# Kernel tuning notes

Measured on AMD Instinct MI355X. Metric: run time of the kernel, lower is better.

## Reference

```python
import jax, jax.numpy as jnp
import numpy as np

B, N, K, D = 16, 16384, 16, 256  # batch, num feature tokens, num slots, slot/feature dim
FEAT = 256
LN_EPS = 1e-5


def _ln(x, g, b):
    m = jnp.mean(x, -1, keepdims=True)
    v = jnp.mean((x - m) ** 2, -1, keepdims=True)
    return (x - m) * jax.lax.rsqrt(v + LN_EPS) * g + b


def setup_inputs() -> dict:
    key = jax.random.key(0)
    ks = jax.random.split(key, 18)
    s = 0.02
    return {
        "features": jax.random.normal(ks[0], (B, N, FEAT), jnp.float32),
        "slots_init": jax.random.normal(ks[1], (B, K, D), jnp.float32),
        "g_f": jnp.ones((FEAT,), jnp.float32), "b_f": jnp.zeros((FEAT,), jnp.float32),
        "g_s": jnp.ones((D,), jnp.float32), "b_s": jnp.zeros((D,), jnp.float32),
        "g_m": jnp.ones((D,), jnp.float32), "b_m": jnp.zeros((D,), jnp.float32),
        "Wq": jax.random.normal(ks[2], (D, D), jnp.float32) * s,
        "Wk": jax.random.normal(ks[3], (D, FEAT), jnp.float32) * s,
        "Wv": jax.random.normal(ks[4], (D, FEAT), jnp.float32) * s,
        "w_ih": jax.random.normal(ks[5], (3 * D, D), jnp.float32) * s,
        "w_hh": jax.random.normal(ks[6], (3 * D, D), jnp.float32) * s,
        "b_ih": jnp.zeros((3 * D,), jnp.float32),
        "b_hh": jnp.zeros((3 * D,), jnp.float32),
        "W1": jax.random.normal(ks[7], (4 * D, D), jnp.float32) * s,
        "b1": jnp.zeros((4 * D,), jnp.float32),
        "W2": jax.random.normal(ks[8], (D, 4 * D), jnp.float32) * s,
        "b2": jnp.zeros((D,), jnp.float32),
        "num_src_view": 4,
    }


def reference(features, slots_init, g_f, b_f, g_s, b_s, g_m, b_m, Wq, Wk, Wv,
              w_ih, w_hh, b_ih, b_hh, W1, b1, W2, b2, num_src_view):
    f = _ln(features, g_f, b_f)            # [B,N,FEAT]
    k = f @ Wk.T                            # [B,N,D]
    v = f @ Wv.T                            # [B,N,D]
    scale = float(D) ** -0.5                # num_head = 1, head-mean is identity

    def gru(x, h):  # PyTorch GRUCell math, batched over [B,K]
        gi = x @ w_ih.T + b_ih
        gh = h @ w_hh.T + b_hh
        ir, iz, inn = jnp.split(gi, 3, -1)
        hr, hz, hn = jnp.split(gh, 3, -1)
        r = jax.nn.sigmoid(ir + hr)
        z = jax.nn.sigmoid(iz + hz)
        n = jnp.tanh(inn + r * hn)
        return (1.0 - z) * n + z * h

    def one_iter(slots):
        q = _ln(slots, g_s, b_s) @ Wq.T                         # [B,K,D]
        logits = jnp.einsum('bkd,bnd->bkn', q, k) * scale       # [B,K,N]
        attn = jax.nn.softmax(logits, axis=1)                   # competitive over slots
        attn_wm = attn / (jnp.sum(attn, -1, keepdims=True) + 1.0)  # epsilon = 1.0
        updates = jnp.einsum('bkn,bnd->bkd', attn_wm, v)        # [B,K,D]
        h = gru(updates, slots)
        h = h + (jax.nn.relu(_ln(h, g_m, b_m) @ W1.T + b1) @ W2.T + b2)
        return h, attn

    slots = slots_init
    for _ in range(2):  # num_iter - 1 iterations with straight-through detach trick
        slots, _ = one_iter(slots)
        slots = jax.lax.stop_gradient(slots) + slots_init - jax.lax.stop_gradient(slots_init)
    slots, attn = one_iter(slots)
    return slots, attn
```

## Files before the change

kernel.cpp:

```cpp
#include <hip/hip_runtime.h>
#include <cstdint>
#include <cstddef>

#define BB    16
#define NTOK  16384
#define KS    16
#define DD    256
#define FEATN 256
#define NBLK  32
#define LN_EPS 1e-5f

typedef float        float4v __attribute__((ext_vector_type(4)));
typedef unsigned int uint4v  __attribute__((ext_vector_type(4)));
typedef unsigned int uint2v  __attribute__((ext_vector_type(2)));
typedef __bf16       bf16x8  __attribute__((ext_vector_type(8)));

__device__ __forceinline__ float bflo(unsigned u){ return __builtin_bit_cast(float, u << 16); }
__device__ __forceinline__ float bfhi(unsigned u){ return __builtin_bit_cast(float, u & 0xffff0000u); }
__device__ __forceinline__ unsigned short f2bf(float v){ __bf16 b = (__bf16)v; return __builtin_bit_cast(unsigned short, b); }
__device__ __forceinline__ float sigm(float x){ return 1.f/(1.f + __expf(-x)); }

__global__ void prep_w_kernel(const float* __restrict__ Wv, const float* __restrict__ w_ih,
                              const float* __restrict__ w_hh, const float* __restrict__ W1,
                              const float* __restrict__ W2, const float* __restrict__ Wq,
                              const float* __restrict__ Wk,
                              unsigned short* __restrict__ Wv_t, unsigned short* __restrict__ wih_t,
                              unsigned short* __restrict__ whh_t, unsigned short* __restrict__ W1_t,
                              unsigned short* __restrict__ W2_t, unsigned short* __restrict__ Wq_t,
                              unsigned short* __restrict__ Wk_b)
{
  __shared__ float tile[64][65];
  const int t = blockIdx.x, tid = threadIdx.x;
  const float* src; unsigned short* dst; int R, C, base;
  if      (t < 16)  { src = Wv;   dst = Wv_t;  R = 256;  C = 256;  base = 0;   }
  else if (t < 64)  { src = w_ih; dst = wih_t; R = 768;  C = 256;  base = 16;  }
  else if (t < 112) { src = w_hh; dst = whh_t; R = 768;  C = 256;  base = 64;  }
  else if (t < 176) { src = W1;   dst = W1_t;  R = 1024; C = 256;  base = 112; }
  else if (t < 240) { src = W2;   dst = W2_t;  R = 256;  C = 1024; base = 176; }
  else if (t < 256) { src = Wq;   dst = Wq_t;  R = 256;  C = 256;  base = 240; }
  else {
    const int t2 = t - 256;
    for (int i = tid; i < 4096; i += 256) {
      const int idx = t2*4096 + i;
      Wk_b[idx] = f2bf(Wk[idx]);
    }
    return;
  }
  const int tt = t - base;
  const int tiles_r = R >> 6;
  const int r0 = (tt % tiles_r) * 64, c0 = (tt / tiles_r) * 64;
  const int j = tid & 63, i0 = (tid >> 6) * 16;
  for (int s = 0; s < 16; ++s)
    tile[i0 + s][j] = src[(size_t)(r0 + i0 + s)*C + c0 + j];
  __syncthreads();
  for (int s = 0; s < 16; ++s) {
    const int i = i0 + s;
    dst[(size_t)(c0 + i)*R + r0 + j] = f2bf(tile[j][i]);
  }
}

__device__ __forceinline__ void lnqu_tail_p(
    const float* Vs, float* Ys, float* Qs, float* Pp, float* SUb, float* CBb,
    const float* __restrict__ g_s, const float* __restrict__ b_s,
    const unsigned short* __restrict__ Wq_t, const unsigned short* __restrict__ Wk_b,
    const float* __restrict__ g_f, const float* __restrict__ b_f,
    unsigned short* __restrict__ u_buf, float* __restrict__ su_buf, float* __restrict__ cb_buf,
    int b, int k0, int tid)
{
  const int w = tid >> 6, L = tid & 63;
  {
    const float v0 = Vs[w*256+L], v1 = Vs[w*256+64+L], v2 = Vs[w*256+128+L], v3 = Vs[w*256+192+L];
    float s = v0+v1+v2+v3;
    #pragma unroll
    for (int m = 1; m < 64; m <<= 1) s += __shfl_xor(s, m);
    const float mean = s * (1.f/DD);
    const float d0 = v0-mean, d1 = v1-mean, d2 = v2-mean, d3 = v3-mean;
    float s2 = d0*d0 + d1*d1 + d2*d2 + d3*d3;
    #pragma unroll
    for (int m = 1; m < 64; m <<= 1) s2 += __shfl_xor(s2, m);
    const float rs = rsqrtf(s2 * (1.f/DD) + LN_EPS);
    Ys[L*4+w]       = d0*rs*g_s[L]      + b_s[L];
    Ys[(64+L)*4+w]  = d1*rs*g_s[64+L]   + b_s[64+L];
    Ys[(128+L)*4+w] = d2*rs*g_s[128+L]  + b_s[128+L];
    Ys[(192+L)*4+w] = d3*rs*g_s[192+L]  + b_s[192+L];
  }
  __syncthreads();
  {
    float acc[4][4] = {};
    for (int cc = w*64; cc < w*64+64; ++cc) {
      const float4v xv = *reinterpret_cast<const float4v*>(Ys + cc*4);
      const uint2v wr = *reinterpret_cast<const uint2v*>(Wq_t + (size_t)cc*DD + 4*L);
      const float w0 = bflo(wr[0]), w1 = bfhi(wr[0]), w2 = bflo(wr[1]), w3 = bfhi(wr[1]);
      #pragma unroll
      for (int s = 0; s < 4; ++s) {
        acc[s][0] += xv[s]*w0; acc[s][1] += xv[s]*w1;
        acc[s][2] += xv[s]*w2; acc[s][3] += xv[s]*w3;
      }
    }
    #pragma unroll
    for (int s = 0; s < 4; ++s)
      *reinterpret_cast<float4v*>(Pp + (w*4+s)*256 + 4*L) = *reinterpret_cast<const float4v*>(acc[s]);
  }
  __syncthreads();
  for (int i = tid; i < 4*DD; i += 256) {
    const int kk = i >> 8, d = i & 255;
    Qs[d*4+kk] = Pp[(0*4+kk)*256+d] + Pp[(1*4+kk)*256+d] + Pp[(2*4+kk)*256+d] + Pp[(3*4+kk)*256+d];
  }
  __syncthreads();
  {
    float acc[4][4] = {};
    for (int d = w*64; d < w*64+64; ++d) {
      const float4v xv = *reinterpret_cast<const float4v*>(Qs + d*4);
      const uint2v wr = *reinterpret_cast<const uint2v*>(Wk_b + (size_t)d*DD + 4*L);
      const float w0 = bflo(wr[0]), w1 = bfhi(wr[0]), w2 = bflo(wr[1]), w3 = bfhi(wr[1]);
      #pragma unroll
      for (int s = 0; s < 4; ++s) {
        acc[s][0] += xv[s]*w0; acc[s][1] += xv[s]*w1;
        acc[s][2] += xv[s]*w2; acc[s][3] += xv[s]*w3;
      }
    }
    #pragma unroll
    for (int s = 0; s < 4; ++s)
      *reinterpret_cast<float4v*>(Pp + (w*4+s)*256 + 4*L) = *reinterpret_cast<const float4v*>(acc[s]);
  }
  __syncthreads();
  for (int i = tid; i < 4*DD; i += 256) {
    const int kk = i >> 8, cc = i & 255;
    const float qk = Pp[(0*4+kk)*256+cc] + Pp[(1*4+kk)*256+cc] + Pp[(2*4+kk)*256+cc] + Pp[(3*4+kk)*256+cc];
    const float uv = qk * g_f[cc];
    u_buf[(size_t)(b*KS + k0 + kk)*DD + cc] = f2bf(uv);
    SUb[kk*256+cc] = uv;
    CBb[kk*256+cc] = qk * b_f[cc];
  }
  __syncthreads();
  {
    float s  = SUb[w*256+L] + SUb[w*256+64+L] + SUb[w*256+128+L] + SUb[w*256+192+L];
    float cv = CBb[w*256+L] + CBb[w*256+64+L] + CBb[w*256+128+L] + CBb[w*256+192+L];
    #pragma unroll
    for (int m = 1; m < 64; m <<= 1) { s += __shfl_xor(s, m); cv += __shfl_xor(cv, m); }
    if (L == 0) { su_buf[b*KS + k0 + w] = s; cb_buf[b*KS + k0 + w] = cv; }
  }
}

__global__ void k0_kernel(const float* __restrict__ slots_init,
                          const float* __restrict__ g_s, const float* __restrict__ b_s,
                          const unsigned short* __restrict__ Wq_t, const unsigned short* __restrict__ Wk_b,
                          const float* __restrict__ g_f, const float* __restrict__ b_f,
                          unsigned short* __restrict__ u_buf, float* __restrict__ su_buf,
                          float* __restrict__ cb_buf)
{
  const int b = blockIdx.x >> 2, k0 = (blockIdx.x & 3) * 4;
  const int tid = threadIdx.x;
  __shared__ __align__(16) float Vs[4*DD];
  __shared__ __align__(16) float Ys[DD*4];
  __shared__ __align__(16) float Qs[DD*4];
  __shared__ __align__(16) float Pp[4*4*DD];
  __shared__ __align__(16) float SUb[4*DD];
  __shared__ __align__(16) float CBb[4*DD];
  for (int i = tid; i < 4*DD; i += 256)
    Vs[i] = slots_init[(size_t)(b*KS + k0)*DD + i];
  __syncthreads();
  lnqu_tail_p(Vs, Ys, Qs, Pp, SUb, CBb, g_s, b_s, Wq_t, Wk_b, g_f, b_f,
              u_buf, su_buf, cb_buf, b, k0, tid);
}

template<int MODE, int LAST>
__launch_bounds__(256, 2)
__global__ void phaseA_kernel(const float* __restrict__ feat,
                              unsigned short* __restrict__ xb, float* __restrict__ stats,
                              const unsigned short* __restrict__ u_buf,
                              const float* __restrict__ su_buf,
                              const float* __restrict__ cb_buf,
                              float* __restrict__ P_part,
                              float* __restrict__ S_part,
                              float* __restrict__ R_part,
                              float* __restrict__ attn_out)
{
  __shared__ __align__(16) unsigned int xl[4][128*36];
  __shared__ float ssh[4][16];
  __shared__ float rsh[4][16];

  const int b   = blockIdx.x / NBLK;
  const int blk = blockIdx.x - b*NBLK;
  const int tid = threadIdx.x;
  const int w = tid >> 6;
  const int l = tid & 63;
  const int c = l & 15;
  const int g = l >> 4;

  bf16x8 ufrag[8];
  {
    const bf16x8* up = reinterpret_cast<const bf16x8*>(u_buf + (size_t)(b*KS + c)*DD);
    #pragma unroll
    for (int kk = 0; kk < 8; ++kk) ufrag[kk] = up[4*kk + g];
  }
  const float su_c = su_buf[b*KS + c];
  const float cb_c = cb_buf[b*KS + c];

  float4v Pacc[16];
  #pragma unroll
  for (int t = 0; t < 16; ++t) Pacc[t] = (float4v){0.f,0.f,0.f,0.f};
  float S_acc = 0.f, R_acc = 0.f;

  unsigned int* myxl = xl[w];
  const int rbase = 8*(c>>2) + (c&3);

  for (int pass = 0; pass < 4; ++pass) {
    const int n0 = blk*(NTOK/NBLK) + pass*128 + w*32;
    float4v Ct[2];
    float m_t[2], rs_t[2];

    if constexpr (MODE == 1) {
      bf16x8 xr0[8], xr1[8];
      float2 st0, st1;
      {
        const size_t row0 = (size_t)b*NTOK + (size_t)(n0 + rbase);
        const size_t row1 = row0 + 4;
        const bf16x8* p0v = reinterpret_cast<const bf16x8*>(xb + row0*FEATN);
        const bf16x8* p1v = reinterpret_cast<const bf16x8*>(xb + row1*FEATN);
        #pragma unroll
        for (int kk = 0; kk < 8; ++kk) { xr0[kk] = p0v[4*kk + g]; xr1[kk] = p1v[4*kk + g]; }
        st0 = *reinterpret_cast<const float2*>(stats + row0*2);
        st1 = *reinterpret_cast<const float2*>(stats + row1*2);
      }
      #pragma unroll
      for (int tp = 0; tp < 2; ++tp) {
        const int nloc = rbase + 4*tp;
        float4v Cacc = (float4v){0.f,0.f,0.f,0.f};
        #pragma unroll
        for (int kk = 0; kk < 8; ++kk) {
          const bf16x8 af = tp ? xr1[kk] : xr0[kk];
          const uint4v ad = __builtin_bit_cast(uint4v, af);
          const int pb = (16*kk + 4*g)*36 + nloc;
          myxl[pb      ] = ad[0];
          myxl[pb + 36 ] = ad[1];
          myxl[pb + 72 ] = ad[2];
          myxl[pb + 108] = ad[3];
          Cacc = __builtin_amdgcn_mfma_f32_16x16x32_bf16(af, ufrag[kk], Cacc, 0, 0, 0);
        }
        m_t[tp]  = tp ? st1.x : st0.x;
        rs_t[tp] = tp ? st1.y : st0.y;
        Ct[tp]   = Cacc;
      }
    } else {
      #pragma unroll
      for (int tp = 0; tp < 2; ++tp) {
        const int nloc = rbase + 4*tp;
        const size_t row = (size_t)b*NTOK + (size_t)(n0 + nloc);
        const float* fr = feat + row*FEATN;
        float4v xf[16];
        #pragma unroll
        for (int kk = 0; kk < 8; ++kk) {
          xf[2*kk]   = *reinterpret_cast<const float4v*>(fr + 32*kk + 8*g);
          xf[2*kk+1] = *reinterpret_cast<const float4v*>(fr + 32*kk + 8*g + 4);
        }
        unsigned short* xw = xb + row*FEATN;
        float sum = 0.f, sq = 0.f;
        float4v Cacc = (float4v){0.f,0.f,0.f,0.f};
        #pragma unroll
        for (int kk = 0; kk < 8; ++kk) {
          const float4v x0 = xf[2*kk], x1 = xf[2*kk+1];
          sum += x0[0]+x0[1]+x0[2]+x0[3] + x1[0]+x1[1]+x1[2]+x1[3];
          sq  += x0[0]*x0[0]+x0[1]*x0[1]+x0[2]*x0[2]+x0[3]*x0[3]
               + x1[0]*x1[0]+x1[1]*x1[1]+x1[2]*x1[2]+x1[3]*x1[3];
          bf16x8 af;
          af[0]=(__bf16)x0[0]; af[1]=(__bf16)x0[1]; af[2]=(__bf16)x0[2]; af[3]=(__bf16)x0[3];
          af[4]=(__bf16)x1[0]; af[5]=(__bf16)x1[1]; af[6]=(__bf16)x1[2]; af[7]=(__bf16)x1[3];
          *reinterpret_cast<bf16x8*>(xw + 32*kk + 8*g) = af;
          const uint4v ad = __builtin_bit_cast(uint4v, af);
          const int pb = (16*kk + 4*g)*36 + nloc;
          myxl[pb      ] = ad[0];
          myxl[pb + 36 ] = ad[1];
          myxl[pb + 72 ] = ad[2];
          myxl[pb + 108] = ad[3];
          Cacc = __builtin_amdgcn_mfma_f32_16x16x32_bf16(af, ufrag[kk], Cacc, 0, 0, 0);
        }
        sum += __shfl_xor(sum,16); sum += __shfl_xor(sum,32);
        sq  += __shfl_xor(sq ,16); sq  += __shfl_xor(sq ,32);
        const float mean = sum * (1.f/FEATN);
        const float var  = sq  * (1.f/FEATN) - mean*mean;
        m_t[tp]  = mean;
        rs_t[tp] = rsqrtf(var + LN_EPS);
        float2 st; st.x = m_t[tp]; st.y = rs_t[tp];
        *reinterpret_cast<float2*>(stats + row*2) = st;
        Ct[tp] = Cacc;
      }
    }

    float arr[8];
    #pragma unroll
    for (int tp = 0; tp < 2; ++tp) {
      float lv[4], rsr[4], mr[4];
      #pragma unroll
      for (int r = 0; r < 4; ++r) {
        const int src = 4*g + r;
        rsr[r] = __shfl(rs_t[tp], src);
        mr[r]  = __shfl(m_t[tp],  src);
        lv[r]  = 0.0625f * (rsr[r]*(Ct[tp][r] - mr[r]*su_c) + cb_c);
      }
      float a_[4];
      #pragma unroll
      for (int r = 0; r < 4; ++r) {
        float v = lv[r];
        v = fmaxf(v, __shfl_xor(v,1));
        v = fmaxf(v, __shfl_xor(v,2));
        v = fmaxf(v, __shfl_xor(v,4));
        v = fmaxf(v, __shfl_xor(v,8));
        const float e = __expf(lv[r] - v);
        float s = e;
        s += __shfl_xor(s,1);
        s += __shfl_xor(s,2);
        s += __shfl_xor(s,4);
        s += __shfl_xor(s,8);
        const float a = e / s;
        a_[r] = a;
        S_acc += a;
        R_acc += a * rsr[r] * mr[r];
        arr[4*tp + r] = a * rsr[r];
      }
      if (LAST) {
        float4v av = {a_[0], a_[1], a_[2], a_[3]};
        *reinterpret_cast<float4v*>(attn_out + (size_t)(b*KS + c)*NTOK + (size_t)(n0 + 8*g + 4*tp)) = av;
      }
    }
    bf16x8 afrag;
    #pragma unroll
    for (int j = 0; j < 8; ++j) afrag[j] = (__bf16)arr[j];

    #pragma unroll
    for (int t = 0; t < 16; ++t) {
      const unsigned int* rp = &myxl[(t*8 + (c>>1))*36 + 8*g];
      const uint4v q0 = *reinterpret_cast<const uint4v*>(rp);
      const uint4v q1 = *reinterpret_cast<const uint4v*>(rp + 4);
      const unsigned int sel = (c & 1) ? 0x07060302u : 0x05040100u;
      uint4v bd;
      bd[0] = __builtin_amdgcn_perm(q0[1], q0[0], sel);
      bd[1] = __builtin_amdgcn_perm(q0[3], q0[2], sel);
      bd[2] = __builtin_amdgcn_perm(q1[1], q1[0], sel);
      bd[3] = __builtin_amdgcn_perm(q1[3], q1[2], sel);
      const bf16x8 bfrag = __builtin_bit_cast(bf16x8, bd);
      Pacc[t] = __builtin_amdgcn_mfma_f32_16x16x32_bf16(afrag, bfrag, Pacc[t], 0, 0, 0);
    }
  }

  S_acc += __shfl_xor(S_acc,16); S_acc += __shfl_xor(S_acc,32);
  R_acc += __shfl_xor(R_acc,16); R_acc += __shfl_xor(R_acc,32);
  if (g == 0) { ssh[w][c] = S_acc; rsh[w][c] = R_acc; }

  float* pf = reinterpret_cast<float*>(myxl);
  #pragma unroll
  for (int t = 0; t < 16; ++t) {
    #pragma unroll
    for (int r = 0; r < 4; ++r) pf[(4*g + r)*256 + t*16 + c] = Pacc[t][r];
  }
  __syncthreads();
  {
    float* outp = P_part + (size_t)blockIdx.x * (KS*DD);
    const float* p0 = reinterpret_cast<const float*>(&xl[0][0]);
    const float* p1 = p0 + 4608;
    const float* p2 = p0 + 9216;
    const float* p3 = p0 + 13824;
    for (int i = tid; i < KS*DD; i += 256) outp[i] = p0[i]+p1[i]+p2[i]+p3[i];
    if (tid < KS) {
      S_part[blockIdx.x*KS + tid] = ssh[0][tid]+ssh[1][tid]+ssh[2][tid]+ssh[3][tid];
      R_part[blockIdx.x*KS + tid] = rsh[0][tid]+rsh[1][tid]+rsh[2][tid]+rsh[3][tid];
    }
  }
}

template<int LAST, int NEXT>
__global__ void fusedB_kernel(const float* __restrict__ P_part, const float* __restrict__ S_part,
                              const float* __restrict__ R_part, const float* __restrict__ slots_in,
                              const float* __restrict__ g_f, const float* __restrict__ b_f,
                              const unsigned short* __restrict__ Wv_t,
                              const unsigned short* __restrict__ wih_t,
                              const unsigned short* __restrict__ whh_t,
                              const float* __restrict__ b_ih, const float* __restrict__ b_hh,
                              const float* __restrict__ g_m, const float* __restrict__ b_m,
                              const unsigned short* __restrict__ W1_t, const float* __restrict__ b1,
                              const unsigned short* __restrict__ W2_t, const float* __restrict__ b2v,
                              const float* __restrict__ g_s, const float* __restrict__ b_s,
                              const unsigned short* __restrict__ Wq_t,
                              const unsigned short* __restrict__ Wk_b,
                              float* __restrict__ slots_next, float* __restrict__ out_slots,
                              unsigned short* __restrict__ u_buf, float* __restrict__ su_buf,
                              float* __restrict__ cb_buf)
{
  const int b = blockIdx.x >> 4, k = blockIdx.x & 15;
  const int tid = threadIdx.x;
  const int w = tid >> 6, L = tid & 63;

  __shared__ __align__(16) float arena[9984];
  __shared__ float SRsh[2];
  __shared__ float redsh[8];

  float* Pp    = arena;
  float* Hsh   = arena + 6144;
  float* Tsh   = arena + 6400;
  float* Ush   = arena + 6656;
  float* Gish  = arena + 6912;
  float* Ghsh  = arena + 7680;
  float* Hpsh  = arena + 8448;
  float* Ysh   = arena + 8704;
  float* Hidsh = arena + 8960;

  Hsh[tid] = slots_in[(size_t)(b*KS + k)*DD + tid];
  if (tid < 64) {
    const int p = tid & 31;
    const float* sp = (tid < 32) ? S_part : R_part;
    float v = sp[(b*NBLK + p)*KS + k];
    v += __shfl_xor(v, 1); v += __shfl_xor(v, 2); v += __shfl_xor(v, 4);
    v += __shfl_xor(v, 8); v += __shfl_xor(v, 16);
    if (p == 0) SRsh[tid >> 5] = v;
  }
  __syncthreads();

  {
    const float S = SRsh[0], R = SRsh[1];
    const float inv = 1.f / (S + 1.f);
    const float* pb = P_part + (size_t)(b*NBLK)*KS*DD + (size_t)k*DD + tid;
    float p0 = 0.f, p1 = 0.f, p2 = 0.f, p3 = 0.f;
    #pragma unroll
    for (int p = 0; p < NBLK; p += 4) {
      p0 += pb[(size_t)(p+0)*KS*DD];
      p1 += pb[(size_t)(p+1)*KS*DD];
      p2 += pb[(size_t)(p+2)*KS*DD];
      p3 += pb[(size_t)(p+3)*KS*DD];
    }
    const float P = (p0 + p1) + (p2 + p3);
    Tsh[tid] = (g_f[tid]*(P - R) + S*b_f[tid]) * inv;
  }
  __syncthreads();

  {
    const int c0 = 4*L;
    float a0 = 0.f, a1 = 0.f, a2 = 0.f, a3 = 0.f;
    for (int cc = w*64; cc < w*64+64; ++cc) {
      const float x = Tsh[cc];
      const uint2v wr = *reinterpret_cast<const uint2v*>(Wv_t + (size_t)cc*DD + c0);
      a0 += x*bflo(wr[0]); a1 += x*bfhi(wr[0]);
      a2 += x*bflo(wr[1]); a3 += x*bfhi(wr[1]);
    }
    float4v av = {a0, a1, a2, a3};
    *reinterpret_cast<float4v*>(Pp + w*256 + c0) = av;
  }
  __syncthreads();
  Ush[tid] = Pp[tid] + Pp[256+tid] + Pp[512+tid] + Pp[768+tid];
  __syncthreads();

  {
    const int c0 = 4*L;
    float ai[3][4] = {}, ah[3][4] = {};
    for (int cc = w*64; cc < w*64+64; ++cc) {
      const float xi = Ush[cc], xh = Hsh[cc];
      #pragma unroll
      for (int c = 0; c < 3; ++c) {
        const uint2v wi = *reinterpret_cast<const uint2v*>(wih_t + (size_t)cc*768 + c0 + 256*c);
        const uint2v wh = *reinterpret_cast<const uint2v*>(whh_t + (size_t)cc*768 + c0 + 256*c);
        ai[c][0] += xi*bflo(wi[0]); ai[c][1] += xi*bfhi(wi[0]);
        ai[c][2] += xi*bflo(wi[1]); ai[c][3] += xi*bfhi(wi[1]);
        ah[c][0] += xh*bflo(wh[0]); ah[c][1] += xh*bfhi(wh[0]);
        ah[c][2] += xh*bflo(wh[1]); ah[c][3] += xh*bfhi(wh[1]);
      }
    }
    #pragma unroll
    for (int c = 0; c < 3; ++c) {
      *reinterpret_cast<float4v*>(Pp + w*768 + 256*c + c0)        = *reinterpret_cast<const float4v*>(ai[c]);
      *reinterpret_cast<float4v*>(Pp + 3072 + w*768 + 256*c + c0) = *reinterpret_cast<const float4v*>(ah[c]);
    }
  }
  __syncthreads();
  for (int j = tid; j < 768; j += 256) {
    Gish[j] = b_ih[j] + Pp[j] + Pp[768+j] + Pp[1536+j] + Pp[2304+j];
    Ghsh[j] = b_hh[j] + Pp[3072+j] + Pp[3840+j] + Pp[4608+j] + Pp[5376+j];
  }
  __syncthreads();

  {
    const int d = tid;
    const float r = sigm(Gish[d] + Ghsh[d]);
    const float z = sigm(Gish[256+d] + Ghsh[256+d]);
    const float n = tanhf(Gish[512+d] + r*Ghsh[512+d]);
    const float hp = (1.f - z)*n + z*Hsh[d];
    Hpsh[d] = hp;
    float s = hp;
    #pragma unroll
    for (int m = 1; m < 64; m <<= 1) s += __shfl_xor(s, m);
    if (L == 0) redsh[w] = s;
    __syncthreads();
    const float mean = (redsh[0]+redsh[1]+redsh[2]+redsh[3]) * (1.f/DD);
    const float dv = hp - mean;
    float s2 = dv*dv;
    #pragma unroll
    for (int m = 1; m < 64; m <<= 1) s2 += __shfl_xor(s2, m);
    if (L == 0) redsh[4+w] = s2;
    __syncthreads();
    const float var = (redsh[4]+redsh[5]+redsh[6]+redsh[7]) * (1.f/DD);
    Ysh[d] = dv * rsqrtf(var + LN_EPS) * g_m[d] + b_m[d];
  }
  __syncthreads();

  {
    const int c0 = 4*L;
    float a[4][4] = {};
    for (int cc = w*64; cc < w*64+64; ++cc) {
      const float x = Ysh[cc];
      #pragma unroll
      for (int c = 0; c < 4; ++c) {
        const uint2v wr = *reinterpret_cast<const uint2v*>(W1_t + (size_t)cc*1024 + c0 + 256*c);
        a[c][0] += x*bflo(wr[0]); a[c][1] += x*bfhi(wr[0]);
        a[c][2] += x*bflo(wr[1]); a[c][3] += x*bfhi(wr[1]);
      }
    }
    #pragma unroll
    for (int c = 0; c < 4; ++c)
      *reinterpret_cast<float4v*>(Pp + w*1024 + 256*c + c0) = *reinterpret_cast<const float4v*>(a[c]);
  }
  __syncthreads();
  for (int j = tid; j < 1024; j += 256)
    Hidsh[j] = fmaxf(b1[j] + Pp[j] + Pp[1024+j] + Pp[2048+j] + Pp[3072+j], 0.f);
  __syncthreads();

  {
    const int c0 = 4*L;
    float a0 = 0.f, a1 = 0.f, a2 = 0.f, a3 = 0.f;
    for (int cc = w*256; cc < w*256+256; ++cc) {
      const float x = Hidsh[cc];
      const uint2v wr = *reinterpret_cast<const uint2v*>(W2_t + (size_t)cc*DD + c0);
      a0 += x*bflo(wr[0]); a1 += x*bfhi(wr[0]);
      a2 += x*bflo(wr[1]); a3 += x*bfhi(wr[1]);
    }
    float4v av = {a0, a1, a2, a3};
    *reinterpret_cast<float4v*>(Pp + w*256 + c0) = av;
  }
  __syncthreads();
  {
    const int d = tid;
    const float v = b2v[d] + Pp[d] + Pp[256+d] + Pp[512+d] + Pp[768+d] + Hpsh[d];
    Tsh[d] = v;
    slots_next[(size_t)(b*KS + k)*DD + d] = v;
    if (LAST) out_slots[(size_t)(b*KS + k)*DD + d] = v;
  }

  if constexpr (NEXT) {
    __syncthreads();
    {
      const float v = Tsh[tid];
      float s = v;
      #pragma unroll
      for (int m = 1; m < 64; m <<= 1) s += __shfl_xor(s, m);
      if (L == 0) redsh[w] = s;
      __syncthreads();
      const float mean = (redsh[0]+redsh[1]+redsh[2]+redsh[3]) * (1.f/DD);
      const float dv = v - mean;
      float s2 = dv*dv;
      #pragma unroll
      for (int m = 1; m < 64; m <<= 1) s2 += __shfl_xor(s2, m);
      if (L == 0) redsh[4+w] = s2;
      __syncthreads();
      const float var = (redsh[4]+redsh[5]+redsh[6]+redsh[7]) * (1.f/DD);
      Ush[tid] = dv * rsqrtf(var + LN_EPS) * g_s[tid] + b_s[tid];
    }
    __syncthreads();
    {
      const int c0 = 4*L;
      float a0 = 0.f, a1 = 0.f, a2 = 0.f, a3 = 0.f;
      for (int cc = w*64; cc < w*64+64; ++cc) {
        const float x = Ush[cc];
        const uint2v wr = *reinterpret_cast<const uint2v*>(Wq_t + (size_t)cc*DD + c0);
        a0 += x*bflo(wr[0]); a1 += x*bfhi(wr[0]);
        a2 += x*bflo(wr[1]); a3 += x*bfhi(wr[1]);
      }
      float4v av = {a0, a1, a2, a3};
      *reinterpret_cast<float4v*>(Pp + w*256 + c0) = av;
    }
    __syncthreads();
    Hsh[tid] = Pp[tid] + Pp[256+tid] + Pp[512+tid] + Pp[768+tid];
    __syncthreads();
    {
      const int c0 = 4*L;
      float a0 = 0.f, a1 = 0.f, a2 = 0.f, a3 = 0.f;
      for (int dd = w*64; dd < w*64+64; ++dd) {
        const float x = Hsh[dd];
        const uint2v wr = *reinterpret_cast<const uint2v*>(Wk_b + (size_t)dd*DD + c0);
        a0 += x*bflo(wr[0]); a1 += x*bfhi(wr[0]);
        a2 += x*bflo(wr[1]); a3 += x*bfhi(wr[1]);
      }
      float4v av = {a0, a1, a2, a3};
      *reinterpret_cast<float4v*>(Pp + w*256 + c0) = av;
    }
    __syncthreads();
    {
      const int cidx = tid;
      const float qk = Pp[cidx] + Pp[256+cidx] + Pp[512+cidx] + Pp[768+cidx];
      const float uv = qk * g_f[cidx];
      u_buf[(size_t)(b*KS + k)*DD + cidx] = f2bf(uv);
      float s  = uv;
      float cv = qk * b_f[cidx];
      #pragma unroll
      for (int m = 1; m < 64; m <<= 1) { s += __shfl_xor(s, m); cv += __shfl_xor(cv, m); }
      if (L == 0) { redsh[w] = s; redsh[4+w] = cv; }
      __syncthreads();
      if (tid == 0) {
        su_buf[b*KS + k] = redsh[0]+redsh[1]+redsh[2]+redsh[3];
        cb_buf[b*KS + k] = redsh[4]+redsh[5]+redsh[6]+redsh[7];
      }
    }
  }
}

extern "C" void kernel_launch(void* const* d_in, const int* in_sizes, int n_in,
                              void* d_out, int out_size, void* d_ws, size_t ws_size,
                              hipStream_t stream)
{
  const float* features   = (const float*)d_in[0];
  const float* slots_init = (const float*)d_in[1];
  const float* g_f = (const float*)d_in[2];
  const float* b_f = (const float*)d_in[3];
  const float* g_s = (const float*)d_in[4];
  const float* b_s = (const float*)d_in[5];
  const float* g_m = (const float*)d_in[6];
  const float* b_m = (const float*)d_in[7];
  const float* Wq  = (const float*)d_in[8];
  const float* Wk  = (const float*)d_in[9];
  const float* Wv  = (const float*)d_in[10];
  const float* w_ih = (const float*)d_in[11];
  const float* w_hh = (const float*)d_in[12];
  const float* b_ih = (const float*)d_in[13];
  const float* b_hh = (const float*)d_in[14];
  const float* W1  = (const float*)d_in[15];
  const float* b1  = (const float*)d_in[16];
  const float* W2  = (const float*)d_in[17];
  const float* b2  = (const float*)d_in[18];

  float* out_slots = (float*)d_out;
  float* out_attn  = out_slots + (size_t)BB*KS*DD;

  char* ws = (char*)d_ws;
  size_t off = 0;
  auto alloc = [&](size_t bytes) -> void* {
    void* p = ws + off;
    off += (bytes + 255) & ~(size_t)255;
    return p;
  };
  unsigned short* u_buf  = (unsigned short*)alloc((size_t)BB*KS*DD*2);
  float*          su_buf = (float*)alloc((size_t)BB*KS*4);
  float*          cb_buf = (float*)alloc((size_t)BB*KS*4);
  float*          P_part = (float*)alloc((size_t)BB*NBLK*KS*DD*4);
  float*          S_part = (float*)alloc((size_t)BB*NBLK*KS*4);
  float*          R_part = (float*)alloc((size_t)BB*NBLK*KS*4);
  float*          slots_ws = (float*)alloc((size_t)BB*KS*DD*4);
  unsigned short* Wv_t  = (unsigned short*)alloc((size_t)256*256*2);
  unsigned short* wih_t = (unsigned short*)alloc((size_t)256*768*2);
  unsigned short* whh_t = (unsigned short*)alloc((size_t)256*768*2);
  unsigned short* W1_t  = (unsigned short*)alloc((size_t)256*1024*2);
  unsigned short* W2_t  = (unsigned short*)alloc((size_t)1024*256*2);
  unsigned short* Wq_t  = (unsigned short*)alloc((size_t)256*256*2);
  unsigned short* Wk_b  = (unsigned short*)alloc((size_t)256*256*2);
  float*          stats = (float*)alloc((size_t)BB*NTOK*2*4);
  unsigned short* xb    = (unsigned short*)alloc((size_t)BB*NTOK*FEATN*2);
  (void)in_sizes; (void)n_in; (void)out_size; (void)ws_size;

  prep_w_kernel<<<272, 256, 0, stream>>>(Wv, w_ih, w_hh, W1, W2, Wq, Wk,
                                         Wv_t, wih_t, whh_t, W1_t, W2_t, Wq_t, Wk_b);
  k0_kernel<<<BB*4, 256, 0, stream>>>(slots_init, g_s, b_s, Wq_t, Wk_b, g_f, b_f,
                                      u_buf, su_buf, cb_buf);

  phaseA_kernel<0,0><<<BB*NBLK, 256, 0, stream>>>(features, xb, stats, u_buf, su_buf, cb_buf,
                                                  P_part, S_part, R_part, out_attn);
  fusedB_kernel<0,1><<<BB*KS, 256, 0, stream>>>(P_part, S_part, R_part, slots_init, g_f, b_f,
                                                Wv_t, wih_t, whh_t, b_ih, b_hh, g_m, b_m,
                                                W1_t, b1, W2_t, b2, g_s, b_s, Wq_t, Wk_b,
                                                slots_ws, out_slots, u_buf, su_buf, cb_buf);
  phaseA_kernel<1,0><<<BB*NBLK, 256, 0, stream>>>(features, xb, stats, u_buf, su_buf, cb_buf,
                                                  P_part, S_part, R_part, out_attn);
  fusedB_kernel<0,1><<<BB*KS, 256, 0, stream>>>(P_part, S_part, R_part, slots_ws, g_f, b_f,
                                                Wv_t, wih_t, whh_t, b_ih, b_hh, g_m, b_m,
                                                W1_t, b1, W2_t, b2, g_s, b_s, Wq_t, Wk_b,
                                                slots_ws, out_slots, u_buf, su_buf, cb_buf);
  phaseA_kernel<1,1><<<BB*NBLK, 256, 0, stream>>>(features, xb, stats, u_buf, su_buf, cb_buf,
                                                  P_part, S_part, R_part, out_attn);
  fusedB_kernel<1,0><<<BB*KS, 256, 0, stream>>>(P_part, S_part, R_part, slots_ws, g_f, b_f,
                                                Wv_t, wih_t, whh_t, b_ih, b_hh, g_m, b_m,
                                                W1_t, b1, W2_t, b2, g_s, b_s, Wq_t, Wk_b,
                                                slots_ws, out_slots, u_buf, su_buf, cb_buf);
}
```

Measured before the change: 390.0 us.

## Fuse phase A and B kernels into one persistent kernel with flag sync

Replaces six alternating phaseA/fusedB launches with a single persistent kernel of 512 blocks. Inside it, per-batch global atomic flags signal when phase A partials are ready and when updated slots are ready, and the first 16 blocks of each batch run the B stage. This removes kernel launch gaps and whole-grid barriers so that different batches can proceed independently. It relies on all 512 blocks being co-resident (2 per CU, 256 CUs) to avoid deadlock, spins on flags, and also reduces the unroll of the partial-sum loop.

Result: slower. 640.4 us (+64.2%).

```diff
diff --git a/kernel.cpp b/kernel.cpp
--- a/kernel.cpp
+++ b/kernel.cpp
@@ -165,24 +165,13 @@
 }
 
 template<int MODE, int LAST>
-__launch_bounds__(256, 2)
-__global__ void phaseA_kernel(const float* __restrict__ feat,
-                              unsigned short* __restrict__ xb, float* __restrict__ stats,
-                              const unsigned short* __restrict__ u_buf,
-                              const float* __restrict__ su_buf,
-                              const float* __restrict__ cb_buf,
-                              float* __restrict__ P_part,
-                              float* __restrict__ S_part,
-                              float* __restrict__ R_part,
-                              float* __restrict__ attn_out)
+__device__ __forceinline__ void phaseA_dev(
+    unsigned int* xl, float* ssh, float* rsh, int b, int blk, int bid, int tid,
+    const float* __restrict__ feat, unsigned short* __restrict__ xb, float* __restrict__ stats,
+    const unsigned short* __restrict__ u_buf, const float* __restrict__ su_buf,
+    const float* __restrict__ cb_buf, float* __restrict__ P_part,
+    float* __restrict__ S_part, float* __restrict__ R_part, float* __restrict__ attn_out)
 {
-  __shared__ __align__(16) unsigned int xl[4][128*36];
-  __shared__ float ssh[4][16];
-  __shared__ float rsh[4][16];
-
-  const int b   = blockIdx.x / NBLK;
-  const int blk = blockIdx.x - b*NBLK;
-  const int tid = threadIdx.x;
   const int w = tid >> 6;
   const int l = tid & 63;
   const int c = l & 15;
@@ -202,7 +191,7 @@
   for (int t = 0; t < 16; ++t) Pacc[t] = (float4v){0.f,0.f,0.f,0.f};
   float S_acc = 0.f, R_acc = 0.f;
 
-  unsigned int* myxl = xl[w];
+  unsigned int* myxl = xl + w*4608;
   const int rbase = 8*(c>>2) + (c&3);
 
   for (int pass = 0; pass < 4; ++pass) {
@@ -345,7 +334,7 @@
 
   S_acc += __shfl_xor(S_acc,16); S_acc += __shfl_xor(S_acc,32);
   R_acc += __shfl_xor(R_acc,16); R_acc += __shfl_xor(R_acc,32);
-  if (g == 0) { ssh[w][c] = S_acc; rsh[w][c] = R_acc; }
+  if (g == 0) { ssh[w*16 + c] = S_acc; rsh[w*16 + c] = R_acc; }
 
   float* pf = reinterpret_cast<float*>(myxl);
   #pragma unroll
@@ -355,45 +344,37 @@
   }
   __syncthreads();
   {
-    float* outp = P_part + (size_t)blockIdx.x * (KS*DD);
-    const float* p0 = reinterpret_cast<const float*>(&xl[0][0]);
+    float* outp = P_part + (size_t)bid * (KS*DD);
+    const float* p0 = reinterpret_cast<const float*>(xl);
     const float* p1 = p0 + 4608;
     const float* p2 = p0 + 9216;
     const float* p3 = p0 + 13824;
     for (int i = tid; i < KS*DD; i += 256) outp[i] = p0[i]+p1[i]+p2[i]+p3[i];
     if (tid < KS) {
-      S_part[blockIdx.x*KS + tid] = ssh[0][tid]+ssh[1][tid]+ssh[2][tid]+ssh[3][tid];
-      R_part[blockIdx.x*KS + tid] = rsh[0][tid]+rsh[1][tid]+rsh[2][tid]+rsh[3][tid];
+      S_part[bid*KS + tid] = ssh[tid]+ssh[16+tid]+ssh[32+tid]+ssh[48+tid];
+      R_part[bid*KS + tid] = rsh[tid]+rsh[16+tid]+rsh[32+tid]+rsh[48+tid];
     }
   }
 }
 
 template<int LAST, int NEXT>
-__global__ void fusedB_kernel(const float* __restrict__ P_part, const float* __restrict__ S_part,
-                              const float* __restrict__ R_part, const float* __restrict__ slots_in,
-                              const float* __restrict__ g_f, const float* __restrict__ b_f,
-                              const unsigned short* __restrict__ Wv_t,
-                              const unsigned short* __restrict__ wih_t,
-                              const unsigned short* __restrict__ whh_t,
-                              const float* __restrict__ b_ih, const float* __restrict__ b_hh,
-                              const float* __restrict__ g_m, const float* __restrict__ b_m,
-                              const unsigned short* __restrict__ W1_t, const float* __restrict__ b1,
-                              const unsigned short* __restrict__ W2_t, const float* __restrict__ b2v,
-                              const float* __restrict__ g_s, const float* __restrict__ b_s,
-                              const unsigned short* __restrict__ Wq_t,
-                              const unsigned short* __restrict__ Wk_b,
-                              float* __restrict__ slots_next, float* __restrict__ out_slots,
-                              unsigned short* __restrict__ u_buf, float* __restrict__ su_buf,
-                              float* __restrict__ cb_buf)
+__device__ __forceinline__ void fusedB_dev(
+    float* arena, float* SRsh, float* redsh, int b, int k, int tid,
+    const float* __restrict__ P_part, const float* __restrict__ S_part,
+    const float* __restrict__ R_part, const float* __restrict__ slots_in,
+    const float* __restrict__ g_f, const float* __restrict__ b_f,
+    const unsigned short* __restrict__ Wv_t, const unsigned short* __restrict__ wih_t,
+    const unsigned short* __restrict__ whh_t,
+    const float* __restrict__ b_ih, const float* __restrict__ b_hh,
+    const float* __restrict__ g_m, const float* __restrict__ b_m,
+    const unsigned short* __restrict__ W1_t, const float* __restrict__ b1,
+    const unsigned short* __restrict__ W2_t, const float* __restrict__ b2v,
+    const float* __restrict__ g_s, const float* __restrict__ b_s,
+    const unsigned short* __restrict__ Wq_t, const unsigned short* __restrict__ Wk_b,
+    float* __restrict__ slots_next, float* __restrict__ out_slots,
+    unsigned short* __restrict__ u_buf, float* __restrict__ su_buf, float* __restrict__ cb_buf)
 {
-  const int b = blockIdx.x >> 4, k = blockIdx.x & 15;
-  const int tid = threadIdx.x;
   const int w = tid >> 6, L = tid & 63;
-
-  __shared__ __align__(16) float arena[9984];
-  __shared__ float SRsh[2];
-  __shared__ float redsh[8];
-
   float* Pp    = arena;
   float* Hsh   = arena + 6144;
   float* Tsh   = arena + 6400;
@@ -420,7 +401,7 @@
     const float inv = 1.f / (S + 1.f);
     const float* pb = P_part + (size_t)(b*NBLK)*KS*DD + (size_t)k*DD + tid;
     float p0 = 0.f, p1 = 0.f, p2 = 0.f, p3 = 0.f;
-    #pragma unroll
+    #pragma unroll 2
     for (int p = 0; p < NBLK; p += 4) {
       p0 += pb[(size_t)(p+0)*KS*DD];
       p1 += pb[(size_t)(p+1)*KS*DD];
@@ -606,6 +587,114 @@
         cb_buf[b*KS + k] = redsh[4]+redsh[5]+redsh[6]+redsh[7];
       }
     }
+  }
+}
+
+__launch_bounds__(256, 2)
+__global__ void giant_kernel(const float* __restrict__ feat,
+                             unsigned short* __restrict__ xb, float* __restrict__ stats,
+                             unsigned short* __restrict__ u_buf,
+                             float* __restrict__ su_buf, float* __restrict__ cb_buf,
+                             float* __restrict__ P_part, float* __restrict__ S_part,
+                             float* __restrict__ R_part, float* __restrict__ attn_out,
+                             const float* __restrict__ slots_init, float* __restrict__ slots_ws,
+                             const float* __restrict__ g_f, const float* __restrict__ b_f,
+                             const unsigned short* __restrict__ Wv_t,
+                             const unsigned short* __restrict__ wih_t,
+                             const unsigned short* __restrict__ whh_t,
+                             const float* __restrict__ b_ih, const float* __restrict__ b_hh,
+                             const float* __restrict__ g_m, const float* __restrict__ b_m,
+                             const unsigned short* __restrict__ W1_t, const float* __restrict__ b1,
+                             const unsigned short* __restrict__ W2_t, const float* __restrict__ b2v,
+                             const float* __restrict__ g_s, const float* __restrict__ b_s,
+                             const unsigned short* __restrict__ Wq_t,
+                             const unsigned short* __restrict__ Wk_b,
+                             float* __restrict__ out_slots,
+                             int* __restrict__ FA, int* __restrict__ FB)
+{
+  __shared__ __align__(16) char smem[74304];
+  unsigned int* xl  = reinterpret_cast<unsigned int*>(smem);
+  float* ssh  = reinterpret_cast<float*>(smem + 73728);
+  float* rsh  = reinterpret_cast<float*>(smem + 73984);
+  float* SRsh = reinterpret_cast<float*>(smem + 74240);
+  float* redsh= reinterpret_cast<float*>(smem + 74248);
+
+  const int bid = blockIdx.x;
+  const int b = bid >> 5, blk = bid & 31;
+  const int tid = threadIdx.x;
+  const bool isfB = (blk < 16);
+  const int k = blk;
+
+  auto signalA = [&](int it) {
+    __syncthreads();
+    if (tid < 16) {
+      __threadfence();
+      atomicExch(&FA[((it*BB + b)*16 + tid)*32 + blk], 1);
+    }
+  };
+  auto waitA = [&](int it) {
+    if (tid < 32) {
+      int* fp = &FA[((it*BB + b)*16 + k)*32 + tid];
+      while (atomicAdd(fp, 0) != 1) { __builtin_amdgcn_s_sleep(2); }
+    }
+    __syncthreads();
+    if (tid < 32) atomicExch(&FA[((it*BB + b)*16 + k)*32 + tid], 0);
+    __threadfence();
+    __syncthreads();
+  };
+  auto signalB = [&](int it) {
+    __syncthreads();
+    if (tid < 32) {
+      __threadfence();
+      atomicExch(&FB[((it*BB + b)*32 + tid)*16 + k], 1);
+    }
+  };
+  auto waitB = [&](int it) {
+    if (tid < 16) {
+      int* fp = &FB[((it*BB + b)*32 + blk)*16 + tid];
+      while (atomicAdd(fp, 0) != 1) { __builtin_amdgcn_s_sleep(2); }
+    }
+    __syncthreads();
+    if (tid < 16) atomicExch(&FB[((it*BB + b)*32 + blk)*16 + tid], 0);
+    __threadfence();
+    __syncthreads();
+  };
+
+  phaseA_dev<0,0>(xl, ssh, rsh, b, blk, bid, tid, feat, xb, stats, u_buf, su_buf, cb_buf,
+                  P_part, S_part, R_part, attn_out);
+  signalA(0);
+  if (isfB) {
+    waitA(0);
+    fusedB_dev<0,1>(reinterpret_cast<float*>(smem), SRsh, redsh, b, k, tid,
+                    P_part, S_part, R_part, slots_init, g_f, b_f, Wv_t, wih_t, whh_t,
+                    b_ih, b_hh, g_m, b_m, W1_t, b1, W2_t, b2v, g_s, b_s, Wq_t, Wk_b,
+                    slots_ws, out_slots, u_buf, su_buf, cb_buf);
+    signalB(0);
+  }
+  waitB(0);
+
+  phaseA_dev<1,0>(xl, ssh, rsh, b, blk, bid, tid, feat, xb, stats, u_buf, su_buf, cb_buf,
+                  P_part, S_part, R_part, attn_out);
+  signalA(1);
+  if (isfB) {
+    waitA(1);
+    fusedB_dev<0,1>(reinterpret_cast<float*>(smem), SRsh, redsh, b, k, tid,
+                    P_part, S_part, R_part, slots_ws, g_f, b_f, Wv_t, wih_t, whh_t,
+                    b_ih, b_hh, g_m, b_m, W1_t, b1, W2_t, b2v, g_s, b_s, Wq_t, Wk_b,
+                    slots_ws, out_slots, u_buf, su_buf, cb_buf);
+    signalB(1);
+  }
+  waitB(1);
+
+  phaseA_dev<1,1>(xl, ssh, rsh, b, blk, bid, tid, feat, xb, stats, u_buf, su_buf, cb_buf,
+                  P_part, S_part, R_part, attn_out);
+  signalA(2);
+  if (isfB) {
+    waitA(2);
+    fusedB_dev<1,0>(reinterpret_cast<float*>(smem), SRsh, redsh, b, k, tid,
+                    P_part, S_part, R_part, slots_ws, g_f, b_f, Wv_t, wih_t, whh_t,
+                    b_ih, b_hh, g_m, b_m, W1_t, b1, W2_t, b2v, g_s, b_s, Wq_t, Wk_b,
+                    slots_ws, out_slots, u_buf, su_buf, cb_buf);
   }
 }
 
@@ -650,6 +739,8 @@
   float*          S_part = (float*)alloc((size_t)BB*NBLK*KS*4);
   float*          R_part = (float*)alloc((size_t)BB*NBLK*KS*4);
   float*          slots_ws = (float*)alloc((size_t)BB*KS*DD*4);
+  int*            FA     = (int*)alloc((size_t)3*BB*16*32*4);
+  int*            FB     = (int*)alloc((size_t)3*BB*32*16*4);
   unsigned short* Wv_t  = (unsigned short*)alloc((size_t)256*256*2);
   unsigned short* wih_t = (unsigned short*)alloc((size_t)256*768*2);
   unsigned short* whh_t = (unsigned short*)alloc((size_t)256*768*2);
@@ -661,27 +752,16 @@
   unsigned short* xb    = (unsigned short*)alloc((size_t)BB*NTOK*FEATN*2);
   (void)in_sizes; (void)n_in; (void)out_size; (void)ws_size;
 
+  hipMemsetAsync(FA, 0, (size_t)3*BB*16*32*4 + (size_t)3*BB*32*16*4 + 512, stream);
+
   prep_w_kernel<<<272, 256, 0, stream>>>(Wv, w_ih, w_hh, W1, W2, Wq, Wk,
                                          Wv_t, wih_t, whh_t, W1_t, W2_t, Wq_t, Wk_b);
   k0_kernel<<<BB*4, 256, 0, stream>>>(slots_init, g_s, b_s, Wq_t, Wk_b, g_f, b_f,
                                       u_buf, su_buf, cb_buf);
-
-  phaseA_kernel<0,0><<<BB*NBLK, 256, 0, stream>>>(features, xb, stats, u_buf, su_buf, cb_buf,
-                                                  P_part, S_part, R_part, out_attn);
-  fusedB_kernel<0,1><<<BB*KS, 256, 0, stream>>>(P_part, S_part, R_part, slots_init, g_f, b_f,
-                                                Wv_t, wih_t, whh_t, b_ih, b_hh, g_m, b_m,
-                                                W1_t, b1, W2_t, b2, g_s, b_s, Wq_t, Wk_b,
-                                                slots_ws, out_slots, u_buf, su_buf, cb_buf);
-  phaseA_kernel<1,0><<<BB*NBLK, 256, 0, stream>>>(features, xb, stats, u_buf, su_buf, cb_buf,
-                                                  P_part, S_part, R_part, out_attn);
-  fusedB_kernel<0,1><<<BB*KS, 256, 0, stream>>>(P_part, S_part, R_part, slots_ws, g_f, b_f,
-                                                Wv_t, wih_t, whh_t, b_ih, b_hh, g_m, b_m,
-                                                W1_t, b1, W2_t, b2, g_s, b_s, Wq_t, Wk_b,
-                                                slots_ws, out_slots, u_buf, su_buf, cb_buf);
-  phaseA_kernel<1,1><<<BB*NBLK, 256, 0, stream>>>(features, xb, stats, u_buf, su_buf, cb_buf,
-                                                  P_part, S_part, R_part, out_attn);
-  fusedB_kernel<1,0><<<BB*KS, 256, 0, stream>>>(P_part, S_part, R_part, slots_ws, g_f, b_f,
-                                                Wv_t, wih_t, whh_t, b_ih, b_hh, g_m, b_m,
-                                                W1_t, b1, W2_t, b2, g_s, b_s, Wq_t, Wk_b,
-                                                slots_ws, out_slots, u_buf, su_buf, cb_buf);
+  giant_kernel<<<BB*NBLK, 256, 0, stream>>>(features, xb, stats, u_buf, su_buf, cb_buf,
+                                            P_part, S_part, R_part, out_attn,
+                                            slots_init, slots_ws, g_f, b_f,
+                                            Wv_t, wih_t, whh_t, b_ih, b_hh, g_m, b_m,
+                                            W1_t, b1, W2_t, b2, g_s, b_s, Wq_t, Wk_b,
+                                            out_slots, FA, FB);
 }
```
